# Kernel tuning notes

Hardware: AMD Instinct MI355X
Metric: run time of the kernel (lower is better)

The kernel has to match this reference:

```python
import jax, jax.numpy as jnp
import numpy as np

H, A, V = 8, 32, 32
NODE_IN, EDGE_IN, NODE_OUT, EDGE_OUT = 128, 64, 128, 64


def setup_inputs() -> dict:
    key = jax.random.key(0)
    ks = jax.random.split(key, 8)
    B, N = 1, 384
    s = lambda fan: 1.0 / np.sqrt(fan).astype(np.float32)
    nodes = jax.random.normal(ks[0], (B, NODE_IN, N), jnp.float32)
    edges = jax.random.normal(ks[1], (B, EDGE_IN, N, N), jnp.float32)
    mask = jax.random.randint(ks[2], (B, N), 0, 2).astype(bool)
    W_q = jax.random.normal(ks[3], (A * H, NODE_IN), jnp.float32) * s(NODE_IN)
    W_k = jax.random.normal(ks[4], (A * H, NODE_IN + EDGE_IN), jnp.float32) * s(NODE_IN + EDGE_IN)
    W_v = jax.random.normal(ks[5], (V * H, NODE_IN + EDGE_IN), jnp.float32) * s(NODE_IN + EDGE_IN)
    W_o = jax.random.normal(ks[6], (NODE_OUT, V * H), jnp.float32) * s(V * H)
    W_e = jax.random.normal(ks[7], (EDGE_OUT, V * H + EDGE_IN), jnp.float32) * s(V * H + EDGE_IN)
    return dict(nodes=nodes, edges=edges, mask=mask, W_q=W_q, W_k=W_k, W_v=W_v, W_o=W_o, W_e=W_e)


def reference(nodes, edges, mask, W_q, W_k, W_v, W_o, W_e):
    B, C, N = nodes.shape
    # 1x1 convs are channel matmuls
    query = jnp.einsum('oc,bcn->bon', W_q, nodes)                      # [B, H*A, N]
    node_edges = jnp.concatenate(
        [jnp.broadcast_to(nodes[:, :, :, None], (B, C, N, N)), edges], axis=1)  # [B, C+E, N, N]
    key = jnp.einsum('oc,bcij->boij', W_k, node_edges)                 # [B, H*A, N, N]
    value = jnp.einsum('oc,bcij->boij', W_v, node_edges).reshape(B, H, V, N, N)
    # elementwise QK: query broadcast over column axis j
    sim = (query[:, :, :, None] * key).reshape(B, H, A, N, N).sum(axis=2)
    sim = sim / jnp.sqrt(jnp.asarray(A, sim.dtype))                    # [B, H, N, N]
    sim = jnp.where(mask[:, None, None, :], sim, -jnp.inf)
    sim = jax.nn.softmax(sim, axis=-1)
    mm = (mask[:, None, :, None] & mask[:, None, None, :]).astype(sim.dtype)  # [B,1,N,N]
    sim = sim * mm
    value = value * mm[:, None]
    node_features = jnp.einsum('bhij,bhvij->bhvi', sim, value).reshape(B, H * V, N)
    node_out = jnp.einsum('od,bdn->bon', W_o, node_features)           # [B, node_out, N]
    # symmetrized edge features: (f_i + f_j) / 2, then concat raw edges
    ef = (node_features[:, :, :, None] + node_features[:, :, None, :]) * 0.5  # [B,H*V,N,N]
    ef = jnp.concatenate([ef, edges], axis=1)
    edge_out = jnp.einsum('oc,bcij->boij', W_e, ef)                    # [B, edge_out, N, N]
    return node_out, edge_out
```

## Files before the change

kernel.cpp:

```cpp
#include <hip/hip_runtime.h>
#include <math.h>

#define NN 384
#define NSQ (NN*NN)

#define WS_MASKF 0
#define WS_C1    384
#define WS_P     3456
#define WS_VN    200064
#define WS_T     298368
#define WS_GH    494976
#define WS_WT    519552
#define WS_WOT   523648
#define WS_WVE   556416
#define WS_WEN   572800

typedef short short8 __attribute__((ext_vector_type(8)));
typedef float f32x4 __attribute__((ext_vector_type(4)));

__device__ __forceinline__ unsigned short f2bf(float x) {
    unsigned u = __float_as_uint(x);
    return (unsigned short)((u + 0x7FFFu + ((u >> 16) & 1u)) >> 16);
}
__device__ __forceinline__ float bf2f(unsigned short b) {
    return __uint_as_float(((unsigned)b) << 16);
}

__global__ __launch_bounds__(256) void k_proj(
    const float* __restrict__ nodes, const float* __restrict__ Wq,
    const float* __restrict__ Wk, const float* __restrict__ Wv,
    const float* __restrict__ Wo, const float* __restrict__ We,
    const unsigned int* __restrict__ mi, float* __restrict__ ws) {
    int tid = threadIdx.x;
    if (blockIdx.x >= 48) {
        if (blockIdx.x == 48) {
            __shared__ int bytemode;
            if (tid == 0) bytemode = 0;
            __syncthreads();
            unsigned v0 = mi[tid];
            unsigned v1 = (tid < 128) ? mi[256 + tid] : 0u;
            if (v0 > 1u || v1 > 1u) bytemode = 1;
            __syncthreads();
            float* maskf = ws + WS_MASKF;
            for (int j = tid; j < NN; j += 256) {
                int on;
                if (bytemode) on = (((const unsigned char*)mi)[j] != 0);
                else          on = (mi[j] != 0u);
                maskf[j] = on ? 1.0f : 0.0f;
            }
        } else if (blockIdx.x == 49) {
            unsigned short* WtBF = reinterpret_cast<unsigned short*>(ws + WS_WT);
            for (int idx = tid; idx < 4096; idx += 256) {
                int o = idx >> 6, c = idx & 63;
                WtBF[o * 64 + c] = f2bf(We[o * 320 + 256 + c]);
            }
        } else if (blockIdx.x == 50) {
            float* WoT = ws + WS_WOT;
            for (int idx = tid; idx < 32768; idx += 256) {
                int dd = idx >> 7, o = idx & 127;
                WoT[dd * 128 + o] = Wo[o * 256 + dd];
            }
        } else if (blockIdx.x == 51) {
            float* WvE = ws + WS_WVE;
            for (int idx = tid; idx < 16384; idx += 256) {
                int c = idx >> 8, d = idx & 255;
                WvE[c * 256 + d] = Wv[d * 192 + 128 + c];
            }
        } else {
            float* WeN = ws + WS_WEN;
            for (int idx = tid; idx < 16384; idx += 256) {
                int dd = idx >> 6, o = idx & 63;
                WeN[dd * 64 + o] = We[o * 320 + dd];
            }
        }
        return;
    }
    float* c1_ws = ws + WS_C1;
    float* P_ws  = ws + WS_P;
    float* vn_ws = ws + WS_VN;
    int i0 = blockIdx.x * 8;
    __shared__ float nl[128][8];
    __shared__ float q_l[256][8];
    __shared__ float qk_l[256][8];
    for (int idx = tid; idx < 1024; idx += 256) {
        int m = idx >> 3, ii = idx & 7;
        nl[m][ii] = nodes[m * NN + i0 + ii];
    }
    __syncthreads();
    int o = tid;
    float aq[8], ak[8], av[8];
#pragma unroll
    for (int ii = 0; ii < 8; ii++) { aq[ii] = 0.f; ak[ii] = 0.f; av[ii] = 0.f; }
#pragma unroll 4
    for (int m = 0; m < 128; m++) {
        float wq = Wq[o * 128 + m];
        float wk = Wk[o * 192 + m];
        float wv = Wv[o * 192 + m];
#pragma unroll
        for (int ii = 0; ii < 8; ii++) {
            float nv = nl[m][ii];
            aq[ii] = fmaf(wq, nv, aq[ii]);
            ak[ii] = fmaf(wk, nv, ak[ii]);
            av[ii] = fmaf(wv, nv, av[ii]);
        }
    }
#pragma unroll
    for (int ii = 0; ii < 8; ii++) {
        vn_ws[(size_t)(i0 + ii) * 256 + o] = av[ii];
        q_l[o][ii]  = aq[ii];
        qk_l[o][ii] = aq[ii] * ak[ii];
    }
    __syncthreads();
    if (tid < 64) {
        int h = tid >> 3, ii = tid & 7;
        float s = 0.f;
        for (int a = 0; a < 32; a++) s += qk_l[h * 32 + a][ii];
        c1_ws[(i0 + ii) * 8 + h] = s;
    }
    for (int rep = 0; rep < 2; rep++) {
        int idx = rep * 256 + tid;
        int c = idx & 63, h = idx >> 6;
        float ap[8];
#pragma unroll
        for (int ii = 0; ii < 8; ii++) ap[ii] = 0.f;
        for (int a = 0; a < 32; a++) {
            float w = Wk[(h * 32 + a) * 192 + 128 + c];
#pragma unroll
            for (int ii = 0; ii < 8; ii++)
                ap[ii] = fmaf(q_l[h * 32 + a][ii], w, ap[ii]);
        }
#pragma unroll
        for (int ii = 0; ii < 8; ii++)
            P_ws[(size_t)(i0 + ii) * 512 + c * 8 + h] = ap[ii];
    }
}

__global__ __launch_bounds__(512) void k_attn(
    const float* __restrict__ edges, const float* __restrict__ ws_ro,
    float* __restrict__ gh_ws, float* __restrict__ out) {
    __shared__ __align__(16) unsigned short epad_h[64 * 392];
    __shared__ __align__(16) float sT2[NN * 8];
    __shared__ __align__(16) float T_lds[512];
    __shared__ float nf_lds[256];
    const float* maskf = ws_ro + WS_MASKF;
    const float* c1w   = ws_ro + WS_C1;
    const float* Pw    = ws_ro + WS_P;
    const float* vn_ws = ws_ro + WS_VN;
    const float* WvE   = ws_ro + WS_WVE;
    const float* WoT   = ws_ro + WS_WOT;
    const float* WeN   = ws_ro + WS_WEN;
    int i = blockIdx.x;
    int tid = threadIdx.x;
    int wv = tid >> 6, ln = tid & 63;
    float mask_i = maskf[i];

    {
        int c = tid >> 3, g = tid & 7;
        const float* src = edges + (size_t)c * NSQ + (size_t)i * NN + g * 48;
        float4 v0  = reinterpret_cast<const float4*>(src)[0];
        float4 v1  = reinterpret_cast<const float4*>(src)[1];
        float4 v2  = reinterpret_cast<const float4*>(src)[2];
        float4 v3  = reinterpret_cast<const float4*>(src)[3];
        float4 v4  = reinterpret_cast<const float4*>(src)[4];
        float4 v5  = reinterpret_cast<const float4*>(src)[5];
        float4 v6  = reinterpret_cast<const float4*>(src)[6];
        float4 v7  = reinterpret_cast<const float4*>(src)[7];
        float4 v8  = reinterpret_cast<const float4*>(src)[8];
        float4 v9  = reinterpret_cast<const float4*>(src)[9];
        float4 v10 = reinterpret_cast<const float4*>(src)[10];
        float4 v11 = reinterpret_cast<const float4*>(src)[11];
        unsigned short* dst = &epad_h[c * 392 + g * 48];
#define PACK2(A, B, OFS)                                                     \
        {                                                                    \
            short8 p;                                                        \
            p[0] = (short)f2bf(A.x); p[1] = (short)f2bf(A.y);                \
            p[2] = (short)f2bf(A.z); p[3] = (short)f2bf(A.w);                \
            p[4] = (short)f2bf(B.x); p[5] = (short)f2bf(B.y);                \
            p[6] = (short)f2bf(B.z); p[7] = (short)f2bf(B.w);                \
            *reinterpret_cast<short8*>(dst + (OFS)) = p;                     \
        }
        PACK2(v0,  v1,  0)
        PACK2(v2,  v3,  8)
        PACK2(v4,  v5,  16)
        PACK2(v6,  v7,  24)
        PACK2(v8,  v9,  32)
        PACK2(v10, v11, 40)
#undef PACK2
    }
    __syncthreads();

    if (tid < NN) {
        int j = tid;
        const float* Pi = Pw + (size_t)i * 512;
        float acc[8];
#pragma unroll
        for (int h = 0; h < 8; h++) acc[h] = 0.f;
#pragma unroll 8
        for (int c = 0; c < 64; c++) {
            float ev = bf2f(epad_h[c * 392 + j]);
            const float* Pc = Pi + c * 8;
#pragma unroll
            for (int h = 0; h < 8; h++) acc[h] = fmaf(Pc[h], ev, acc[h]);
        }
        float mj = maskf[j];
        const float* c1i = c1w + i * 8;
        float sv[8];
#pragma unroll
        for (int h = 0; h < 8; h++) {
            float s = (c1i[h] + acc[h]) * 0.17677669529663687f;
            sv[h] = (mj != 0.0f) ? s : -1e30f;
        }
        *reinterpret_cast<float4*>(&sT2[j * 8])     = make_float4(sv[0], sv[1], sv[2], sv[3]);
        *reinterpret_cast<float4*>(&sT2[j * 8 + 4]) = make_float4(sv[4], sv[5], sv[6], sv[7]);
    }
    __syncthreads();
    float v[6];
    {
        int h = wv;
#pragma unroll
        for (int k = 0; k < 6; k++) v[k] = sT2[(ln + 64 * k) * 8 + h];
    }
    __syncthreads();
    {
        int h = wv;
        float m = v[0];
#pragma unroll
        for (int k = 1; k < 6; k++) m = fmaxf(m, v[k]);
#pragma unroll
        for (int s = 1; s < 64; s <<= 1) m = fmaxf(m, __shfl_xor(m, s));
        float ex[6]; float sum = 0.f;
#pragma unroll
        for (int k = 0; k < 6; k++) { ex[k] = __expf(v[k] - m); sum += ex[k]; }
#pragma unroll
        for (int s = 1; s < 64; s <<= 1) sum += __shfl_xor(sum, s);
        float fac = mask_i / sum;
        unsigned short* s_bf = reinterpret_cast<unsigned short*>(sT2);
#pragma unroll
        for (int k = 0; k < 6; k++)
            s_bf[h * 392 + ln + 64 * k] = f2bf(ex[k] * fac);
    }
    __syncthreads();
    if (tid < 256) {
        const unsigned short* s_bf = reinterpret_cast<const unsigned short*>(sT2);
        int nc   = ln & 15;
        int quad = ln >> 4;
        int hrow = nc & 7;
        f32x4 acc = {0.f, 0.f, 0.f, 0.f};
#pragma unroll
        for (int s = 0; s < 12; s++) {
            int jb = s * 32 + quad * 8;
            short8 a = *reinterpret_cast<const short8*>(&s_bf[hrow * 392 + jb]);
            short8 b = *reinterpret_cast<const short8*>(&epad_h[(wv * 16 + nc) * 392 + jb]);
            acc = __builtin_amdgcn_mfma_f32_16x16x32_bf16(a, b, acc, 0, 0, 0);
        }
        if (ln < 32) {
#pragma unroll
            for (int r = 0; r < 4; r++) {
                int h = quad * 4 + r;
                T_lds[h * 64 + wv * 16 + nc] = acc[r];
            }
        }
    }
    __syncthreads();
    if (tid < 256) {
        int d = tid, h = d >> 5;
        float a0 = 0.f, a1 = 0.f, a2 = 0.f, a3 = 0.f;
#pragma unroll
        for (int c = 0; c < 64; c += 4) {
            a0 = fmaf(WvE[(c    ) * 256 + d], T_lds[h * 64 + c    ], a0);
            a1 = fmaf(WvE[(c + 1) * 256 + d], T_lds[h * 64 + c + 1], a1);
            a2 = fmaf(WvE[(c + 2) * 256 + d], T_lds[h * 64 + c + 2], a2);
            a3 = fmaf(WvE[(c + 3) * 256 + d], T_lds[h * 64 + c + 3], a3);
        }
        nf_lds[d] = mask_i * vn_ws[(size_t)i * 256 + d] + ((a0 + a1) + (a2 + a3));
    }
    __syncthreads();
    if (tid < 128) {
        int o = tid;
        float b0 = 0.f, b1 = 0.f, b2 = 0.f, b3 = 0.f;
#pragma unroll 8
        for (int dd = 0; dd < 256; dd += 4) {
            b0 = fmaf(WoT[(dd    ) * 128 + o], nf_lds[dd    ], b0);
            b1 = fmaf(WoT[(dd + 1) * 128 + o], nf_lds[dd + 1], b1);
            b2 = fmaf(WoT[(dd + 2) * 128 + o], nf_lds[dd + 2], b2);
            b3 = fmaf(WoT[(dd + 3) * 128 + o], nf_lds[dd + 3], b3);
        }
        out[o * NN + i] = (b0 + b1) + (b2 + b3);
    } else if (tid < 192) {
        int o = tid - 128;
        float b0 = 0.f, b1 = 0.f, b2 = 0.f, b3 = 0.f;
#pragma unroll 8
        for (int dd = 0; dd < 256; dd += 4) {
            b0 = fmaf(WeN[(dd    ) * 64 + o], nf_lds[dd    ], b0);
            b1 = fmaf(WeN[(dd + 1) * 64 + o], nf_lds[dd + 1], b1);
            b2 = fmaf(WeN[(dd + 2) * 64 + o], nf_lds[dd + 2], b2);
            b3 = fmaf(WeN[(dd + 3) * 64 + o], nf_lds[dd + 3], b3);
        }
        gh_ws[o * NN + i] = 0.5f * ((b0 + b1) + (b2 + b3));
    }
}

__global__ __launch_bounds__(192) void k_edge(
    const float* __restrict__ edges, const float* __restrict__ ws_ro,
    float* __restrict__ out_e) {
    __shared__ __align__(16) unsigned short eT[96 * 72];
    const unsigned short* WtBF = reinterpret_cast<const unsigned short*>(ws_ro + WS_WT);
    const float* gh = ws_ro + WS_GH;
    int i = blockIdx.x, jh = blockIdx.y, tid = threadIdx.x;

    {
        int c = tid / 3, g = tid - c * 3;
        const float* src = edges + (size_t)c * NSQ + (size_t)i * NN + jh * 96 + g * 32;
        float4 v0 = reinterpret_cast<const float4*>(src)[0];
        float4 v1 = reinterpret_cast<const float4*>(src)[1];
        float4 v2 = reinterpret_cast<const float4*>(src)[2];
        float4 v3 = reinterpret_cast<const float4*>(src)[3];
        float4 v4 = reinterpret_cast<const float4*>(src)[4];
        float4 v5 = reinterpret_cast<const float4*>(src)[5];
        float4 v6 = reinterpret_cast<const float4*>(src)[6];
        float4 v7 = reinterpret_cast<const float4*>(src)[7];
        int j0 = g * 32;
#define SCAT4(V, T)                                                          \
        eT[(j0 + (T) * 4 + 0) * 72 + c] = f2bf(V.x);                         \
        eT[(j0 + (T) * 4 + 1) * 72 + c] = f2bf(V.y);                         \
        eT[(j0 + (T) * 4 + 2) * 72 + c] = f2bf(V.z);                         \
        eT[(j0 + (T) * 4 + 3) * 72 + c] = f2bf(V.w);
        SCAT4(v0, 0) SCAT4(v1, 1) SCAT4(v2, 2) SCAT4(v3, 3)
        SCAT4(v4, 4) SCAT4(v5, 5) SCAT4(v6, 6) SCAT4(v7, 7)
#undef SCAT4
    }
    __syncthreads();

    int L = tid & 63, wv = tid >> 6;
    int nc = L & 15, quad = L >> 4;
    short8 a00 = *reinterpret_cast<const short8*>(&WtBF[(0 * 16 + nc) * 64 + 0  + quad * 8]);
    short8 a01 = *reinterpret_cast<const short8*>(&WtBF[(0 * 16 + nc) * 64 + 32 + quad * 8]);
    short8 a10 = *reinterpret_cast<const short8*>(&WtBF[(1 * 16 + nc) * 64 + 0  + quad * 8]);
    short8 a11 = *reinterpret_cast<const short8*>(&WtBF[(1 * 16 + nc) * 64 + 32 + quad * 8]);
    short8 a20 = *reinterpret_cast<const short8*>(&WtBF[(2 * 16 + nc) * 64 + 0  + quad * 8]);
    short8 a21 = *reinterpret_cast<const short8*>(&WtBF[(2 * 16 + nc) * 64 + 32 + quad * 8]);
    short8 a30 = *reinterpret_cast<const short8*>(&WtBF[(3 * 16 + nc) * 64 + 0  + quad * 8]);
    short8 a31 = *reinterpret_cast<const short8*>(&WtBF[(3 * 16 + nc) * 64 + 32 + quad * 8]);
    float ghi[16];
#pragma unroll
    for (int ot = 0; ot < 4; ot++)
#pragma unroll
        for (int r = 0; r < 4; r++)
            ghi[ot * 4 + r] = gh[(ot * 16 + quad * 4 + r) * NN + i];

#pragma unroll
    for (int jj = 0; jj < 2; jj++) {
        int jt = wv * 2 + jj;
        short8 b0 = *reinterpret_cast<const short8*>(&eT[(jt * 16 + nc) * 72 + 0  + quad * 8]);
        short8 b1 = *reinterpret_cast<const short8*>(&eT[(jt * 16 + nc) * 72 + 32 + quad * 8]);
        int j = jh * 96 + jt * 16 + nc;
        f32x4 c0 = {0.f, 0.f, 0.f, 0.f};
        f32x4 c1 = {0.f, 0.f, 0.f, 0.f};
        f32x4 c2 = {0.f, 0.f, 0.f, 0.f};
        f32x4 c3 = {0.f, 0.f, 0.f, 0.f};
        c0 = __builtin_amdgcn_mfma_f32_16x16x32_bf16(a00, b0, c0, 0, 0, 0);
        c0 = __builtin_amdgcn_mfma_f32_16x16x32_bf16(a01, b1, c0, 0, 0, 0);
        c1 = __builtin_amdgcn_mfma_f32_16x16x32_bf16(a10, b0, c1, 0, 0, 0);
        c1 = __builtin_amdgcn_mfma_f32_16x16x32_bf16(a11, b1, c1, 0, 0, 0);
        c2 = __builtin_amdgcn_mfma_f32_16x16x32_bf16(a20, b0, c2, 0, 0, 0);
        c2 = __builtin_amdgcn_mfma_f32_16x16x32_bf16(a21, b1, c2, 0, 0, 0);
        c3 = __builtin_amdgcn_mfma_f32_16x16x32_bf16(a30, b0, c3, 0, 0, 0);
        c3 = __builtin_amdgcn_mfma_f32_16x16x32_bf16(a31, b1, c3, 0, 0, 0);
#pragma unroll
        for (int ot = 0; ot < 4; ot++) {
            f32x4 cc = ot == 0 ? c0 : ot == 1 ? c1 : ot == 2 ? c2 : c3;
#pragma unroll
            for (int r = 0; r < 4; r++) {
                int o = ot * 16 + quad * 4 + r;
                float val = cc[r] + ghi[ot * 4 + r] + gh[o * NN + j];
                __builtin_nontemporal_store(val, &out_e[(size_t)o * NSQ + (size_t)i * NN + j]);
            }
        }
    }
}

extern "C" void kernel_launch(void* const* d_in, const int* in_sizes, int n_in,
                              void* d_out, int out_size, void* d_ws, size_t ws_size,
                              hipStream_t stream) {
    const float* nodes = (const float*)d_in[0];
    const float* edges = (const float*)d_in[1];
    const unsigned int* mask = (const unsigned int*)d_in[2];
    const float* Wq = (const float*)d_in[3];
    const float* Wk = (const float*)d_in[4];
    const float* Wv = (const float*)d_in[5];
    const float* Wo = (const float*)d_in[6];
    const float* We = (const float*)d_in[7];
    float* out = (float*)d_out;
    float* ws  = (float*)d_ws;
    float* out_e = out + 128 * NN;

    hipLaunchKernelGGL(k_proj, dim3(53), dim3(256), 0, stream,
                       nodes, Wq, Wk, Wv, Wo, We, mask, ws);
    hipLaunchKernelGGL(k_attn, dim3(384), dim3(512), 0, stream,
                       edges, ws, ws + WS_GH, out);
    hipLaunchKernelGGL(k_edge, dim3(384, 4), dim3(192), 0, stream,
                       edges, ws, out_e);
}
```

Before: 156.3 us.

## Fuse edge MFMA GEMM into attention launch and add gh in separate pass

Merges the edge-projection GEMM blocks into the attention kernel's grid so both run concurrently, with a shared 64KB LDS buffer. Since the gh terms come from the attention blocks, the edge blocks write raw GEMM results to out_e, and a new kernel reads out_e back, adds gh_i + gh_j and rewrites it. This overlaps the edge GEMM with attention but adds a full extra read and write of the 64x384x384 fp32 edge output. It also raises the attention kernel's LDS footprint for every block, which may lower occupancy.

```diff
diff --git a/kernel.cpp b/kernel.cpp
--- a/kernel.cpp
+++ b/kernel.cpp
@@ -135,13 +135,62 @@
     }
 }
 
-__global__ __launch_bounds__(512) void k_attn(
+__global__ __launch_bounds__(512) void k_fused(
     const float* __restrict__ edges, const float* __restrict__ ws_ro,
-    float* __restrict__ gh_ws, float* __restrict__ out) {
-    __shared__ __align__(16) unsigned short epad_h[64 * 392];
-    __shared__ __align__(16) float sT2[NN * 8];
-    __shared__ __align__(16) float T_lds[512];
-    __shared__ float nf_lds[256];
+    float* __restrict__ gh_ws, float* __restrict__ out,
+    float* __restrict__ out_e) {
+    __shared__ __align__(16) unsigned char smem[65536];
+    int bx = blockIdx.x;
+    int tid = threadIdx.x;
+
+    if (bx >= 384) {
+        unsigned short* eT = reinterpret_cast<unsigned short*>(smem);
+        const unsigned short* WtBF = reinterpret_cast<const unsigned short*>(ws_ro + WS_WT);
+        int m = bx - 384, i = m >> 2, jh = m & 3;
+        {
+            int c = tid >> 3, g = tid & 7;
+            const float* src = edges + (size_t)c * NSQ + (size_t)i * NN + jh * 96 + g * 12;
+            float4 v0 = reinterpret_cast<const float4*>(src)[0];
+            float4 v1 = reinterpret_cast<const float4*>(src)[1];
+            float4 v2 = reinterpret_cast<const float4*>(src)[2];
+            int j0 = g * 12;
+#define SCAT4(V, T)                                                          \
+            eT[(j0 + (T) * 4 + 0) * 72 + c] = f2bf(V.x);                     \
+            eT[(j0 + (T) * 4 + 1) * 72 + c] = f2bf(V.y);                     \
+            eT[(j0 + (T) * 4 + 2) * 72 + c] = f2bf(V.z);                     \
+            eT[(j0 + (T) * 4 + 3) * 72 + c] = f2bf(V.w);
+            SCAT4(v0, 0) SCAT4(v1, 1) SCAT4(v2, 2)
+#undef SCAT4
+        }
+        __syncthreads();
+        int L = tid & 63, wv = tid >> 6;
+        int nc = L & 15, quad = L >> 4;
+#pragma unroll
+        for (int pp = 0; pp < 3; pp++) {
+            int p = wv * 3 + pp;
+            int jt = p >> 2, ot = p & 3;
+            short8 a0 = *reinterpret_cast<const short8*>(&WtBF[(ot * 16 + nc) * 64 + 0  + quad * 8]);
+            short8 a1 = *reinterpret_cast<const short8*>(&WtBF[(ot * 16 + nc) * 64 + 32 + quad * 8]);
+            short8 b0 = *reinterpret_cast<const short8*>(&eT[(jt * 16 + nc) * 72 + 0  + quad * 8]);
+            short8 b1 = *reinterpret_cast<const short8*>(&eT[(jt * 16 + nc) * 72 + 32 + quad * 8]);
+            f32x4 acc = {0.f, 0.f, 0.f, 0.f};
+            acc = __builtin_amdgcn_mfma_f32_16x16x32_bf16(a0, b0, acc, 0, 0, 0);
+            acc = __builtin_amdgcn_mfma_f32_16x16x32_bf16(a1, b1, acc, 0, 0, 0);
+            int j = jh * 96 + jt * 16 + nc;
+#pragma unroll
+            for (int r = 0; r < 4; r++) {
+                int o = ot * 16 + quad * 4 + r;
+                __builtin_nontemporal_store(acc[r],
+                    &out_e[(size_t)o * NSQ + (size_t)i * NN + j]);
+            }
+        }
+        return;
+    }
+
+    unsigned short* epad_h = reinterpret_cast<unsigned short*>(smem);
+    float* sT2    = reinterpret_cast<float*>(smem + 50176);
+    float* T_lds  = reinterpret_cast<float*>(smem + 62464);
+    float* nf_lds = reinterpret_cast<float*>(smem + 64512);
     const float* maskf = ws_ro + WS_MASKF;
     const float* c1w   = ws_ro + WS_C1;
     const float* Pw    = ws_ro + WS_P;
@@ -149,8 +198,7 @@
     const float* WvE   = ws_ro + WS_WVE;
     const float* WoT   = ws_ro + WS_WOT;
     const float* WeN   = ws_ro + WS_WEN;
-    int i = blockIdx.x;
-    int tid = threadIdx.x;
+    int i = bx;
     int wv = tid >> 6, ln = tid & 63;
     float mask_i = maskf[i];
 
@@ -300,82 +348,23 @@
     }
 }
 
-__global__ __launch_bounds__(192) void k_edge(
-    const float* __restrict__ edges, const float* __restrict__ ws_ro,
-    float* __restrict__ out_e) {
-    __shared__ __align__(16) unsigned short eT[96 * 72];
-    const unsigned short* WtBF = reinterpret_cast<const unsigned short*>(ws_ro + WS_WT);
+__global__ __launch_bounds__(384) void k_edge2(
+    const float* __restrict__ ws_ro, float* __restrict__ out_e) {
     const float* gh = ws_ro + WS_GH;
-    int i = blockIdx.x, jh = blockIdx.y, tid = threadIdx.x;
-
-    {
-        int c = tid / 3, g = tid - c * 3;
-        const float* src = edges + (size_t)c * NSQ + (size_t)i * NN + jh * 96 + g * 32;
-        float4 v0 = reinterpret_cast<const float4*>(src)[0];
-        float4 v1 = reinterpret_cast<const float4*>(src)[1];
-        float4 v2 = reinterpret_cast<const float4*>(src)[2];
-        float4 v3 = reinterpret_cast<const float4*>(src)[3];
-        float4 v4 = reinterpret_cast<const float4*>(src)[4];
-        float4 v5 = reinterpret_cast<const float4*>(src)[5];
-        float4 v6 = reinterpret_cast<const float4*>(src)[6];
-        float4 v7 = reinterpret_cast<const float4*>(src)[7];
-        int j0 = g * 32;
-#define SCAT4(V, T)                                                          \
-        eT[(j0 + (T) * 4 + 0) * 72 + c] = f2bf(V.x);                         \
-        eT[(j0 + (T) * 4 + 1) * 72 + c] = f2bf(V.y);                         \
-        eT[(j0 + (T) * 4 + 2) * 72 + c] = f2bf(V.z);                         \
-        eT[(j0 + (T) * 4 + 3) * 72 + c] = f2bf(V.w);
-        SCAT4(v0, 0) SCAT4(v1, 1) SCAT4(v2, 2) SCAT4(v3, 3)
-        SCAT4(v4, 4) SCAT4(v5, 5) SCAT4(v6, 6) SCAT4(v7, 7)
-#undef SCAT4
-    }
-    __syncthreads();
-
-    int L = tid & 63, wv = tid >> 6;
-    int nc = L & 15, quad = L >> 4;
-    short8 a00 = *reinterpret_cast<const short8*>(&WtBF[(0 * 16 + nc) * 64 + 0  + quad * 8]);
-    short8 a01 = *reinterpret_cast<const short8*>(&WtBF[(0 * 16 + nc) * 64 + 32 + quad * 8]);
-    short8 a10 = *reinterpret_cast<const short8*>(&WtBF[(1 * 16 + nc) * 64 + 0  + quad * 8]);
-    short8 a11 = *reinterpret_cast<const short8*>(&WtBF[(1 * 16 + nc) * 64 + 32 + quad * 8]);
-    short8 a20 = *reinterpret_cast<const short8*>(&WtBF[(2 * 16 + nc) * 64 + 0  + quad * 8]);
-    short8 a21 = *reinterpret_cast<const short8*>(&WtBF[(2 * 16 + nc) * 64 + 32 + quad * 8]);
-    short8 a30 = *reinterpret_cast<const short8*>(&WtBF[(3 * 16 + nc) * 64 + 0  + quad * 8]);
-    short8 a31 = *reinterpret_cast<const short8*>(&WtBF[(3 * 16 + nc) * 64 + 32 + quad * 8]);
-    float ghi[16];
-#pragma unroll
-    for (int ot = 0; ot < 4; ot++)
-#pragma unroll
-        for (int r = 0; r < 4; r++)
-            ghi[ot * 4 + r] = gh[(ot * 16 + quad * 4 + r) * NN + i];
-
-#pragma unroll
-    for (int jj = 0; jj < 2; jj++) {
-        int jt = wv * 2 + jj;
-        short8 b0 = *reinterpret_cast<const short8*>(&eT[(jt * 16 + nc) * 72 + 0  + quad * 8]);
-        short8 b1 = *reinterpret_cast<const short8*>(&eT[(jt * 16 + nc) * 72 + 32 + quad * 8]);
-        int j = jh * 96 + jt * 16 + nc;
-        f32x4 c0 = {0.f, 0.f, 0.f, 0.f};
-        f32x4 c1 = {0.f, 0.f, 0.f, 0.f};
-        f32x4 c2 = {0.f, 0.f, 0.f, 0.f};
-        f32x4 c3 = {0.f, 0.f, 0.f, 0.f};
-        c0 = __builtin_amdgcn_mfma_f32_16x16x32_bf16(a00, b0, c0, 0, 0, 0);
-        c0 = __builtin_amdgcn_mfma_f32_16x16x32_bf16(a01, b1, c0, 0, 0, 0);
-        c1 = __builtin_amdgcn_mfma_f32_16x16x32_bf16(a10, b0, c1, 0, 0, 0);
-        c1 = __builtin_amdgcn_mfma_f32_16x16x32_bf16(a11, b1, c1, 0, 0, 0);
-        c2 = __builtin_amdgcn_mfma_f32_16x16x32_bf16(a20, b0, c2, 0, 0, 0);
-        c2 = __builtin_amdgcn_mfma_f32_16x16x32_bf16(a21, b1, c2, 0, 0, 0);
-        c3 = __builtin_amdgcn_mfma_f32_16x16x32_bf16(a30, b0, c3, 0, 0, 0);
-        c3 = __builtin_amdgcn_mfma_f32_16x16x32_bf16(a31, b1, c3, 0, 0, 0);
-#pragma unroll
-        for (int ot = 0; ot < 4; ot++) {
-            f32x4 cc = ot == 0 ? c0 : ot == 1 ? c1 : ot == 2 ? c2 : c3;
-#pragma unroll
-            for (int r = 0; r < 4; r++) {
-                int o = ot * 16 + quad * 4 + r;
-                float val = cc[r] + ghi[ot * 4 + r] + gh[o * NN + j];
-                __builtin_nontemporal_store(val, &out_e[(size_t)o * NSQ + (size_t)i * NN + j]);
-            }
-        }
+    int i = blockIdx.x, og = blockIdx.y, j = threadIdx.x;
+    float pv[8], gj[8];
+#pragma unroll
+    for (int t = 0; t < 8; t++) {
+        int o = og * 8 + t;
+        pv[t] = out_e[(size_t)o * NSQ + (size_t)i * NN + j];
+        gj[t] = gh[o * NN + j];
+    }
+#pragma unroll
+    for (int t = 0; t < 8; t++) {
+        int o = og * 8 + t;
+        float gi = gh[o * NN + i];
+        __builtin_nontemporal_store((pv[t] + gi) + gj[t],
+            &out_e[(size_t)o * NSQ + (size_t)i * NN + j]);
     }
 }
 
@@ -396,8 +385,8 @@
 
     hipLaunchKernelGGL(k_proj, dim3(53), dim3(256), 0, stream,
                        nodes, Wq, Wk, Wv, Wo, We, mask, ws);
-    hipLaunchKernelGGL(k_attn, dim3(384), dim3(512), 0, stream,
-                       edges, ws, ws + WS_GH, out);
-    hipLaunchKernelGGL(k_edge, dim3(384, 4), dim3(192), 0, stream,
-                       edges, ws, out_e);
-}
+    hipLaunchKernelGGL(k_fused, dim3(1920), dim3(512), 0, stream,
+                       edges, ws, ws + WS_GH, out, out_e);
+    hipLaunchKernelGGL(k_edge2, dim3(384, 8), dim3(384), 0, stream,
+                       ws, out_e);
+}
```

Measured after the change: 166.4 us. 6.5% more time.
